# Optimization experiments

Measured on AMD Instinct MI355X. Metric: run time of the kernel, lower is better.

## Reference

```python
import jax, jax.numpy as jnp
import numpy as np

B, N, C, OUT, KD, H, E = 16, 10000, 256, 256, 16, 4, 320000
NIT = 3
DV = OUT // H  # per-head value dim = 64


def setup_inputs() -> dict:
    key = jax.random.key(0)
    ks = jax.random.split(key, 7)
    x = jax.random.normal(ks[0], (B, N, C), dtype=jnp.float32)
    edge_rows = jax.random.randint(ks[1], (E,), 0, N, dtype=jnp.int32)
    edge_cols = jax.random.randint(ks[2], (E,), 0, N, dtype=jnp.int32)
    edge_vals = jax.random.uniform(ks[3], (E,), dtype=jnp.float32)
    s = 1.0 / np.sqrt(C).astype(np.float32)
    # nn.Linear(C, out, bias=False) computes x @ W.T; we store W already transposed as [C, out]
    Wk = jax.random.uniform(ks[4], (C, KD * H), dtype=jnp.float32, minval=-s, maxval=s)
    Wq = jax.random.uniform(ks[5], (C, KD * H), dtype=jnp.float32, minval=-s, maxval=s)
    Wv = jax.random.uniform(ks[6], (C, OUT), dtype=jnp.float32, minval=-s, maxval=s)
    ln_gamma = jnp.ones((DV,), dtype=jnp.float32)
    ln_beta = jnp.zeros((DV,), dtype=jnp.float32)
    return {"x": x, "edge_vals": edge_vals, "Wk": Wk, "Wq": Wq, "Wv": Wv,
            "ln_gamma": ln_gamma, "ln_beta": ln_beta,
            "edge_rows": edge_rows, "edge_cols": edge_cols}


def reference(x, edge_vals, Wk, Wq, Wv, ln_gamma, ln_beta, edge_rows, edge_cols):
    decay = jnp.linspace(0.1, 0.5, H).astype(x.dtype)[None, None, :, None]  # [1,1,H,1]
    k = jax.nn.elu(x @ Wk) + 1.0          # [B, N, H*KD]
    q = jax.nn.elu(x @ Wq) + 1.0          # [B, N, H*KD]
    v = x @ Wv                            # [B, N, OUT]
    k = k.reshape(B, N, H, KD).transpose(1, 0, 2, 3)  # [N, B, H, KD]
    acc = k
    it = k
    for _ in range(1, NIT):
        it = it * decay                                   # per-head decay
        flat = it.reshape(N, B * H * KD)                  # [N, B*H*KD]
        # sparse mm: out[r] += val * flat[c] for each edge (r, c)
        flat = jax.ops.segment_sum(edge_vals[:, None] * flat[edge_cols],
                                   edge_rows, num_segments=N)
        it = flat.reshape(N, B, H, KD)
        acc = acc + it
    k = acc.transpose(1, 0, 2, 3)                         # [B, N, H, KD]
    w = (k * q.reshape(B, N, H, KD)).mean(-1, keepdims=True)  # [B, N, H, 1]
    v = v.reshape(B, N, H, DV) * w
    mu = v.mean(-1, keepdims=True)
    var = jnp.var(v, axis=-1, keepdims=True)  # biased, as torch LayerNorm
    v = (v - mu) * jax.lax.rsqrt(var + 1e-5) * ln_gamma + ln_beta
    # faithful to torch: reshape [B,N,H,DV] row-major into [N,B,OUT], then swap axes
    out = v.reshape(N, B, OUT).swapaxes(0, 1)
    return out
```

## Files before the change

kernel.cpp:

```cpp
#include <hip/hip_runtime.h>

#define NROW 160000
#define Nn 10000
#define NSTRIPE 1250
#define GRID 256

typedef __attribute__((ext_vector_type(8))) short short8;
typedef __attribute__((ext_vector_type(4))) float float4v;

__device__ __forceinline__ short f2bf(float f) {
  unsigned u = __builtin_bit_cast(unsigned, f);
  u = (u + 0x7FFFu + ((u >> 16) & 1u)) >> 16;
  return (short)u;
}

__device__ __forceinline__ unsigned f2bf2(float a, float b) {
  unsigned ua = __builtin_bit_cast(unsigned, a);
  unsigned ub = __builtin_bit_cast(unsigned, b);
  ua = (ua + 0x7FFFu + ((ua >> 16) & 1u)) >> 16;
  ub = (ub + 0x7FFFu + ((ub >> 16) & 1u));
  return (ua & 0xFFFFu) | (ub & 0xFFFF0000u);
}

__device__ __forceinline__ short8 cvt8(float4 a, float4 b) {
  union { unsigned u[4]; short8 s; } r;
  r.u[0] = f2bf2(a.x, a.y);
  r.u[1] = f2bf2(a.z, a.w);
  r.u[2] = f2bf2(b.x, b.y);
  r.u[3] = f2bf2(b.z, b.w);
  return r.s;
}

__global__ __launch_bounds__(256) void prep_k(const float* __restrict__ Wv,
                                              short* __restrict__ bt) {
  const int n = blockIdx.x, k = threadIdx.x;
  bt[n * 256 + k] = f2bf(Wv[k * 256 + n]);
}

__global__ __launch_bounds__(512, 2) void gemm_ln(const float* __restrict__ x,
                                                  const short* __restrict__ bt,
                                                  const float* __restrict__ gamma,
                                                  const float* __restrict__ beta,
                                                  float* __restrict__ out) {
  __shared__ short blds[65536];
  const int t = threadIdx.x;
  const int w = t >> 6;
  const int gHalf = w >> 2;
  const int h = w & 3;
  const int l = t & 63;
  const int r = l & 15;
  const int q = l >> 4;
  const int xk = r & 7;

  float4 xa[3][4][2];
  int s = blockIdx.x;
  auto LOADX = [&](int sm, int cc, float4 (*dst)[2]) {
    const float* p = x + (size_t)(sm * 128 + gHalf * 64 + r) * 256 + cc * 32 + q * 8;
#pragma unroll
    for (int i = 0; i < 4; ++i) {
      dst[i][0] = *(const float4*)(p + i * 4096);
      dst[i][1] = *(const float4*)(p + i * 4096 + 4);
    }
  };
  LOADX(s, 0, xa[0]);
  LOADX(s, 1, xa[1]);

  for (int i = t; i < 256 * 32; i += 512) {
    const int n = i >> 5, gr = i & 31;
    const int4 v = *(const int4*)(bt + n * 256 + gr * 8);
    *(int4*)&blds[n * 256 + ((gr ^ (n & 7)) << 3)] = v;
  }
  __syncthreads();

  float gm[4], be[4];
#pragma unroll
  for (int j = 0; j < 4; ++j) {
    gm[j] = gamma[j * 16 + r];
    be[j] = beta[j * 16 + r];
  }

  const short* bfb = blds + (h * 64 + r) * 256;
  const int q4 = q * 4;

  for (; s < NSTRIPE; s += GRID) {
    float4v acc[4][4];
#pragma unroll
    for (int i = 0; i < 4; ++i)
#pragma unroll
      for (int j = 0; j < 4; ++j) acc[i][j] = (float4v){0.f, 0.f, 0.f, 0.f};

#pragma unroll
    for (int cc = 0; cc < 8; ++cc) {
      if (cc < 6) LOADX(s, cc + 2, xa[(cc + 2) % 3]);
      short8 af[4], bf[4];
#pragma unroll
      for (int i = 0; i < 4; ++i)
        af[i] = cvt8(xa[cc % 3][i][0], xa[cc % 3][i][1]);
#pragma unroll
      for (int j = 0; j < 4; ++j)
        bf[j] = *(const short8*)&bfb[j * 4096 + (((cc * 4 + q) ^ xk) << 3)];
#pragma unroll
      for (int i = 0; i < 4; ++i)
#pragma unroll
        for (int j = 0; j < 4; ++j)
          acc[i][j] = __builtin_amdgcn_mfma_f32_16x16x32_bf16(af[i], bf[j],
                                                              acc[i][j], 0, 0, 0);
    }

    if (s + GRID < NSTRIPE) {
      LOADX(s + GRID, 0, xa[0]);
      LOADX(s + GRID, 1, xa[1]);
    }

    const int m0 = s * 128 + gHalf * 64;
#pragma unroll
    for (int i = 0; i < 4; ++i) {
#pragma unroll
      for (int reg = 0; reg < 4; ++reg) {
        float s1 = acc[i][0][reg] + acc[i][1][reg] + acc[i][2][reg] + acc[i][3][reg];
        float s2 = acc[i][0][reg] * acc[i][0][reg] + acc[i][1][reg] * acc[i][1][reg] +
                   acc[i][2][reg] * acc[i][2][reg] + acc[i][3][reg] * acc[i][3][reg];
        s1 += __shfl_xor(s1, 1); s2 += __shfl_xor(s2, 1);
        s1 += __shfl_xor(s1, 2); s2 += __shfl_xor(s2, 2);
        s1 += __shfl_xor(s1, 4); s2 += __shfl_xor(s2, 4);
        s1 += __shfl_xor(s1, 8); s2 += __shfl_xor(s2, 8);
        const float mu = s1 * (1.f / 64.f);
        const float var = s2 * (1.f / 64.f) - mu * mu;
        const float inv = rsqrtf(var + 1e-5f);
        const int m = m0 + i * 16 + q4 + reg;
        const int b = m / Nn;
        const int n = m - b * Nn;
        const size_t obase = (size_t)(n & 15) * 2560000u +
                             (size_t)(b * 625 + (n >> 4)) * 256u + h * 64 + r;
#pragma unroll
        for (int j = 0; j < 4; ++j)
          out[obase + j * 16] = (acc[i][j][reg] - mu) * inv * gm[j] + be[j];
      }
    }
  }
}

extern "C" void kernel_launch(void* const* d_in, const int* in_sizes, int n_in,
                              void* d_out, int out_size, void* d_ws, size_t ws_size,
                              hipStream_t stream) {
  const float* x = (const float*)d_in[0];
  const float* Wv = (const float*)d_in[4];
  const float* gamma = (const float*)d_in[5];
  const float* beta = (const float*)d_in[6];
  float* out = (float*)d_out;
  short* wv_bt = (short*)d_ws;

  prep_k<<<256, 256, 0, stream>>>(Wv, wv_bt);
  gemm_ln<<<GRID, 512, 0, stream>>>(x, wv_bt, gamma, beta, out);
}
```

Measured before the change: 365.6 us.

## Replace persistent GEMM loop with one-tile-per-block grid and direct LDS loads

Drops the persistent 256-block grid that looped over stripes with a triple-buffered x prefetch. It now launches one 512-thread block per 128-row tile, and each wave computes a full 16x256 output slice. The pre-swizzle of Wv moves into the prep kernel, so B can be copied straight into LDS with global_load_lds, with no register round-trip. Each block reloads the full 128KB B tile, 1250 times in total instead of 256, and x is loaded all at once with no software pipelining. In return it gets more blocks to hide latency and simpler code.

```diff
diff --git a/kernel.cpp b/kernel.cpp
--- a/kernel.cpp
+++ b/kernel.cpp
@@ -1,9 +1,7 @@
 #include <hip/hip_runtime.h>
 
-#define NROW 160000
+#define Mm 160000
 #define Nn 10000
-#define NSTRIPE 1250
-#define GRID 256
 
 typedef __attribute__((ext_vector_type(8))) short short8;
 typedef __attribute__((ext_vector_type(4))) float float4v;
@@ -31,10 +29,17 @@
   return r.s;
 }
 
+__device__ __forceinline__ void gload_lds16(const void* g, void* l) {
+  __builtin_amdgcn_global_load_lds(
+      (const __attribute__((address_space(1))) unsigned*)g,
+      (__attribute__((address_space(3))) unsigned*)l, 16, 0, 0);
+}
+
 __global__ __launch_bounds__(256) void prep_k(const float* __restrict__ Wv,
                                               short* __restrict__ bt) {
   const int n = blockIdx.x, k = threadIdx.x;
-  bt[n * 256 + k] = f2bf(Wv[k * 256 + n]);
+  const int ksrc = (k & 0xC7) | ((((k >> 3) ^ n) & 7) << 3);
+  bt[n * 256 + k] = f2bf(Wv[ksrc * 256 + n]);
 }
 
 __global__ __launch_bounds__(512, 2) void gemm_ln(const float* __restrict__ x,
@@ -42,100 +47,80 @@
                                                   const float* __restrict__ gamma,
                                                   const float* __restrict__ beta,
                                                   float* __restrict__ out) {
-  __shared__ short blds[65536];
+  __shared__ short Bt[256][256];
   const int t = threadIdx.x;
   const int w = t >> 6;
-  const int gHalf = w >> 2;
-  const int h = w & 3;
   const int l = t & 63;
-  const int r = l & 15;
+  const int c16 = l & 15;
   const int q = l >> 4;
-  const int xk = r & 7;
+  const int xk = c16 & 7;
+  const int m0 = blockIdx.x * 128;
+  const int row = m0 + w * 16 + c16;
 
-  float4 xa[3][4][2];
-  int s = blockIdx.x;
-  auto LOADX = [&](int sm, int cc, float4 (*dst)[2]) {
-    const float* p = x + (size_t)(sm * 128 + gHalf * 64 + r) * 256 + cc * 32 + q * 8;
+  float4 xa[8][2];
+  const float* xp = x + (size_t)row * 256 + q * 8;
 #pragma unroll
-    for (int i = 0; i < 4; ++i) {
-      dst[i][0] = *(const float4*)(p + i * 4096);
-      dst[i][1] = *(const float4*)(p + i * 4096 + 4);
-    }
-  };
-  LOADX(s, 0, xa[0]);
-  LOADX(s, 1, xa[1]);
-
-  for (int i = t; i < 256 * 32; i += 512) {
-    const int n = i >> 5, gr = i & 31;
-    const int4 v = *(const int4*)(bt + n * 256 + gr * 8);
-    *(int4*)&blds[n * 256 + ((gr ^ (n & 7)) << 3)] = v;
-  }
-  __syncthreads();
-
-  float gm[4], be[4];
-#pragma unroll
-  for (int j = 0; j < 4; ++j) {
-    gm[j] = gamma[j * 16 + r];
-    be[j] = beta[j * 16 + r];
+  for (int cc = 0; cc < 8; ++cc) {
+    xa[cc][0] = *(const float4*)(xp + cc * 32);
+    xa[cc][1] = *(const float4*)(xp + cc * 32 + 4);
   }
 
-  const short* bfb = blds + (h * 64 + r) * 256;
-  const int q4 = q * 4;
+#pragma unroll
+  for (int r = 0; r < 16; ++r)
+    gload_lds16(bt + (size_t)r * 4096 + t * 8,
+                (char*)&Bt[0][0] + r * 8192 + w * 1024);
 
-  for (; s < NSTRIPE; s += GRID) {
-    float4v acc[4][4];
+  asm volatile("s_waitcnt vmcnt(0)\n\ts_barrier" ::: "memory");
+
+  float4v acc[16];
 #pragma unroll
-    for (int i = 0; i < 4; ++i)
-#pragma unroll
-      for (int j = 0; j < 4; ++j) acc[i][j] = (float4v){0.f, 0.f, 0.f, 0.f};
+  for (int j = 0; j < 16; ++j) acc[j] = (float4v){0.f, 0.f, 0.f, 0.f};
 
 #pragma unroll
-    for (int cc = 0; cc < 8; ++cc) {
-      if (cc < 6) LOADX(s, cc + 2, xa[(cc + 2) % 3]);
-      short8 af[4], bf[4];
+  for (int cc = 0; cc < 8; ++cc) {
+    const int a = cc >> 1, b = cc & 1;
+    const short8 af = cvt8(xa[cc][0], xa[cc][1]);
+    const int gi = a * 8 + (((b << 2) + q) ^ xk);
 #pragma unroll
-      for (int i = 0; i < 4; ++i)
-        af[i] = cvt8(xa[cc % 3][i][0], xa[cc % 3][i][1]);
+    for (int j = 0; j < 16; ++j) {
+      const short8 bf = *(const short8*)&Bt[j * 16 + c16][gi * 8];
+      acc[j] = __builtin_amdgcn_mfma_f32_16x16x32_bf16(af, bf, acc[j], 0, 0, 0);
+    }
+  }
+
+  float gm[4], bb[4];
 #pragma unroll
-      for (int j = 0; j < 4; ++j)
-        bf[j] = *(const short8*)&bfb[j * 4096 + (((cc * 4 + q) ^ xk) << 3)];
+  for (int jj = 0; jj < 4; ++jj) {
+    gm[jj] = gamma[jj * 16 + c16];
+    bb[jj] = beta[jj * 16 + c16];
+  }
+  const int q4 = q * 4;
 #pragma unroll
-      for (int i = 0; i < 4; ++i)
+  for (int h = 0; h < 4; ++h) {
 #pragma unroll
-        for (int j = 0; j < 4; ++j)
-          acc[i][j] = __builtin_amdgcn_mfma_f32_16x16x32_bf16(af[i], bf[j],
-                                                              acc[i][j], 0, 0, 0);
-    }
-
-    if (s + GRID < NSTRIPE) {
-      LOADX(s + GRID, 0, xa[0]);
-      LOADX(s + GRID, 1, xa[1]);
-    }
-
-    const int m0 = s * 128 + gHalf * 64;
+    for (int reg = 0; reg < 4; ++reg) {
+      float s1 = acc[4 * h + 0][reg] + acc[4 * h + 1][reg] +
+                 acc[4 * h + 2][reg] + acc[4 * h + 3][reg];
+      float s2 = acc[4 * h + 0][reg] * acc[4 * h + 0][reg] +
+                 acc[4 * h + 1][reg] * acc[4 * h + 1][reg] +
+                 acc[4 * h + 2][reg] * acc[4 * h + 2][reg] +
+                 acc[4 * h + 3][reg] * acc[4 * h + 3][reg];
+      s1 += __shfl_xor(s1, 1); s2 += __shfl_xor(s2, 1);
+      s1 += __shfl_xor(s1, 2); s2 += __shfl_xor(s2, 2);
+      s1 += __shfl_xor(s1, 4); s2 += __shfl_xor(s2, 4);
+      s1 += __shfl_xor(s1, 8); s2 += __shfl_xor(s2, 8);
+      const float mu = s1 * (1.f / 64.f);
+      const float var = s2 * (1.f / 64.f) - mu * mu;
+      const float inv = rsqrtf(var + 1e-5f);
+      const int m = m0 + w * 16 + q4 + reg;
+      const int b = m / Nn;
+      const int n = m - b * Nn;
+      const size_t obase = (size_t)(n & 15) * 2560000u +
+                           (size_t)(b * 625 + (n >> 4)) * 256u + h * 64 + c16;
 #pragma unroll
-    for (int i = 0; i < 4; ++i) {
-#pragma unroll
-      for (int reg = 0; reg < 4; ++reg) {
-        float s1 = acc[i][0][reg] + acc[i][1][reg] + acc[i][2][reg] + acc[i][3][reg];
-        float s2 = acc[i][0][reg] * acc[i][0][reg] + acc[i][1][reg] * acc[i][1][reg] +
-                   acc[i][2][reg] * acc[i][2][reg] + acc[i][3][reg] * acc[i][3][reg];
-        s1 += __shfl_xor(s1, 1); s2 += __shfl_xor(s2, 1);
-        s1 += __shfl_xor(s1, 2); s2 += __shfl_xor(s2, 2);
-        s1 += __shfl_xor(s1, 4); s2 += __shfl_xor(s2, 4);
-        s1 += __shfl_xor(s1, 8); s2 += __shfl_xor(s2, 8);
-        const float mu = s1 * (1.f / 64.f);
-        const float var = s2 * (1.f / 64.f) - mu * mu;
-        const float inv = rsqrtf(var + 1e-5f);
-        const int m = m0 + i * 16 + q4 + reg;
-        const int b = m / Nn;
-        const int n = m - b * Nn;
-        const size_t obase = (size_t)(n & 15) * 2560000u +
-                             (size_t)(b * 625 + (n >> 4)) * 256u + h * 64 + r;
-#pragma unroll
-        for (int j = 0; j < 4; ++j)
-          out[obase + j * 16] = (acc[i][j][reg] - mu) * inv * gm[j] + be[j];
-      }
+      for (int jj = 0; jj < 4; ++jj)
+        out[obase + jj * 16] =
+            (acc[4 * h + jj][reg] - mu) * inv * gm[jj] + bb[jj];
     }
   }
 }
@@ -151,5 +136,5 @@
   short* wv_bt = (short*)d_ws;
 
   prep_k<<<256, 256, 0, stream>>>(Wv, wv_bt);
-  gemm_ln<<<GRID, 512, 0, stream>>>(x, wv_bt, gamma, beta, out);
+  gemm_ln<<<Mm / 128, 512, 0, stream>>>(x, wv_bt, gamma, beta, out);
 }
```

Measured after the change: 323.7 us. 1.13x faster.
